# Performance work log

Hardware: AMD Instinct MI355X
Metric: run time of the kernel (lower is better)

Reference implementation:

```python
import jax, jax.numpy as jnp
import numpy as np

N, E, ND, ED, H, OUT, L, VC = 10000, 160000, 8, 4, 128, 256, 6, 6
HEADS, C = 4, 128  # GATConv: out_channels=128 per head, concat=False -> mean over heads


def _ln(x, g, b, eps=1e-5):
    m = x.mean(-1, keepdims=True)
    v = ((x - m) ** 2).mean(-1, keepdims=True)
    return (x - m) * jax.lax.rsqrt(v + eps) * g + b


def _gat_layer(h, src, dst, e_attr, lw, a_src, a_dst, lew, a_edge, bias):
    # h: [N,H]; e_attr: [Etot,H]; PyG GATConv(heads=4, concat=False, edge_dim=H)
    xh = (h @ lw).reshape(N, HEADS, C)                 # [N,4,128]
    eh = (e_attr @ lew).reshape(-1, HEADS, C)          # [Etot,4,128]
    al_s = jnp.einsum('nhc,hc->nh', xh, a_src)
    al_d = jnp.einsum('nhc,hc->nh', xh, a_dst)
    al_e = jnp.einsum('ehc,hc->eh', eh, a_edge)
    alpha = jax.nn.leaky_relu(al_s[src] + al_d[dst] + al_e, 0.2)  # [Etot,4]
    amax = jax.ops.segment_max(alpha, dst, num_segments=N)
    ex = jnp.exp(alpha - amax[dst])
    den = jax.ops.segment_sum(ex, dst, num_segments=N)
    w = ex / (den[dst] + 1e-16)
    out = jax.ops.segment_sum(xh[src] * w[..., None], dst, num_segments=N)  # [N,4,128]
    return out.mean(axis=1) + bias


def setup_inputs() -> dict:
    key = jax.random.key(0)
    ks = jax.random.split(key, 32)
    s = 0.05
    d = {
        'x': jax.random.normal(ks[0], (N, ND), jnp.float32),
        'edge_index': jax.random.randint(ks[1], (2, E), 0, N),
        'edge_attr': jax.random.uniform(ks[2], (E, ED), jnp.float32),
        'vnf_context': jax.random.normal(ks[3], (1, VC), jnp.float32),
        # node embedding
        'node_w': jax.random.normal(ks[4], (ND, H)) * s, 'node_b': jnp.zeros((H,)),
        # EdgeAttentionLayer
        'ea_proj_w': jax.random.normal(ks[5], (ED, H)) * s, 'ea_proj_b': jnp.zeros((H,)),
        'vnf_w': jax.random.normal(ks[6], (VC, H)) * s, 'vnf_b': jnp.zeros((H,)),
        'att1_w': jax.random.normal(ks[7], (2 * H, H)) * s, 'att1_b': jnp.zeros((H,)),
        'att2_w': jax.random.normal(ks[8], (H, H // 2)) * s, 'att2_b': jnp.zeros((H // 2,)),
        'att3_w': jax.random.normal(ks[9], (H // 2, 1)) * s, 'att3_b': jnp.zeros((1,)),
        # per-layer GATConv params (stacked over L layers)
        'gat_lin_w': jax.random.normal(ks[10], (L, H, HEADS * C)) * s,
        'gat_att_src': jax.random.normal(ks[11], (L, HEADS, C)) * s,
        'gat_att_dst': jax.random.normal(ks[12], (L, HEADS, C)) * s,
        'gat_lin_edge_w': jax.random.normal(ks[13], (L, H, HEADS * C)) * s,
        'gat_att_edge': jax.random.normal(ks[14], (L, HEADS, C)) * s,
        'gat_bias': jnp.zeros((L, C)),
        'ln_scale': jnp.ones((L, H)), 'ln_bias': jnp.zeros((L, H)),
        # output projection
        'out_w': jax.random.normal(ks[15], (H, OUT)) * s, 'out_b': jnp.zeros((OUT,)),
    }
    return d


def reference(x, edge_index, edge_attr, vnf_context, node_w, node_b, ea_proj_w, ea_proj_b,
              vnf_w, vnf_b, att1_w, att1_b, att2_w, att2_b, att3_w, att3_b,
              gat_lin_w, gat_att_src, gat_att_dst, gat_lin_edge_w, gat_att_edge, gat_bias,
              ln_scale, ln_bias, out_w, out_b):
    src, dst = edge_index[0], edge_index[1]
    h = x @ node_w + node_b                                   # [N,128]
    # EdgeAttentionLayer (eval mode, no network_state)
    ef = edge_attr @ ea_proj_w + ea_proj_b                    # [E,128]
    vnf = vnf_context @ vnf_w + vnf_b                         # [1,128]
    comb = jnp.concatenate([ef, jnp.broadcast_to(vnf, (E, H))], axis=-1)
    a = jax.nn.relu(comb @ att1_w + att1_b)
    a = jax.nn.relu(a @ att2_w + att2_b)
    e_gate = jax.nn.sigmoid(a @ att3_w + att3_b)              # [E,1]
    w_edge = ef * e_gate                                      # [E,128]
    # GATConv default add_self_loops=True, fill_value='mean'
    loop = jnp.arange(N)
    src2 = jnp.concatenate([src, loop])
    dst2 = jnp.concatenate([dst, loop])
    e2 = jnp.concatenate([w_edge, jnp.broadcast_to(w_edge.mean(0, keepdims=True), (N, H))], axis=0)
    for l in range(L):
        hc = _gat_layer(h, src2, dst2, e2, gat_lin_w[l], gat_att_src[l], gat_att_dst[l],
                        gat_lin_edge_w[l], gat_att_edge[l], gat_bias[l])
        h = _ln(h + jax.nn.relu(hc), ln_scale[l], ln_bias[l])
    return h @ out_w + out_b                                  # [N,256]
```

## Files before the change

kernel.cpp:

```cpp
#include <hip/hip_runtime.h>
#include <hip/hip_bf16.h>
#include <math.h>

#define Nn 10000
#define Ee 160000
#define ET 170000
#define LL 6

typedef short v8s __attribute__((ext_vector_type(8)));
typedef float v4f __attribute__((ext_vector_type(4)));
typedef float v2f __attribute__((ext_vector_type(2)));

__device__ __forceinline__ unsigned short f2bf(float v) {
    unsigned int b = __float_as_uint(v);
    b += 0x7fffu + ((b >> 16) & 1u);
    return (unsigned short)(b >> 16);
}
__device__ __forceinline__ float bflo(unsigned int u) { return __uint_as_float(u << 16); }
__device__ __forceinline__ float bfhi(unsigned int u) { return __uint_as_float(u & 0xffff0000u); }

__global__ void k_node_embed(const float* __restrict__ x, const float* __restrict__ nw,
                             const float* __restrict__ nb, float* __restrict__ h,
                             unsigned short* __restrict__ hb) {
    int idx = blockIdx.x * 256 + threadIdx.x;
    if (idx >= Nn * 128) return;
    int n = idx >> 7, c = idx & 127;
    const float* xr = x + (size_t)n * 8;
    float acc = nb[c];
#pragma unroll
    for (int k = 0; k < 8; k++) acc += xr[k] * nw[k * 128 + c];
    h[idx] = acc;
    hb[idx] = f2bf(acc);
}

__global__ void k_small(const float* __restrict__ vnfc, const float* __restrict__ vw,
                        const float* __restrict__ vb, const float* __restrict__ eab,
                        const float* __restrict__ a1w, const float* __restrict__ a1b,
                        const float* __restrict__ eaw, float* __restrict__ E1) {
    __shared__ float vr[128];
    __shared__ float sM1[512];
    __shared__ float sd1[128];
    int t = threadIdx.x;
    if (t < 128) {
        float a = vb[t];
#pragma unroll
        for (int k = 0; k < 6; k++) a += vnfc[k] * vw[k * 128 + t];
        vr[t] = a;
    }
    __syncthreads();
    if (t < 128) {
        float a = a1b[t];
        for (int k = 0; k < 128; k++) a += eab[k] * a1w[k * 128 + t];
        for (int k = 0; k < 128; k++) a += vr[k] * a1w[(128 + k) * 128 + t];
        sd1[t] = a;
    }
    {
        int r = t >> 7, j = t & 127;
        float a = 0.f;
        for (int k = 0; k < 128; k++) a += eaw[r * 128 + k] * a1w[k * 128 + j];
        sM1[r * 128 + j] = a;
    }
    __syncthreads();
    if (t < 128) {
        E1[t * 8 + 0] = sM1[t];
        E1[t * 8 + 1] = sM1[128 + t];
        E1[t * 8 + 2] = sM1[256 + t];
        E1[t * 8 + 3] = sM1[384 + t];
        E1[t * 8 + 4] = sd1[t];
        E1[t * 8 + 5] = 0.f; E1[t * 8 + 6] = 0.f; E1[t * 8 + 7] = 0.f;
    }
}

__global__ void k_bmat(const float* __restrict__ glw, const float* __restrict__ gas,
                       const float* __restrict__ gad, const float* __restrict__ glew,
                       const float* __restrict__ gae, float* __restrict__ Bs,
                       float* __restrict__ Bd, float* __restrict__ Be) {
    int idx = blockIdx.x * 256 + threadIdx.x;
    if (idx >= LL * 128 * 4) return;
    int hh = idx & 3, k = (idx >> 2) & 127, l = idx >> 9;
    const float* lwp = glw  + (size_t)l * 65536 + k * 512 + hh * 128;
    const float* lep = glew + (size_t)l * 65536 + k * 512 + hh * 128;
    const float* sp = gas + l * 512 + hh * 128;
    const float* dp = gad + l * 512 + hh * 128;
    const float* ep = gae + l * 512 + hh * 128;
    float s1 = 0, s2 = 0, s3 = 0;
    for (int c = 0; c < 128; c++) {
        float lv = lwp[c];
        s1 += lv * sp[c];
        s2 += lv * dp[c];
        s3 += lep[c] * ep[c];
    }
    Bs[idx] = s1; Bd[idx] = s2; Be[idx] = s3;
}

__global__ void k_wsum(const float* __restrict__ glw, unsigned short* __restrict__ WsumT) {
    int idx = blockIdx.x * 256 + threadIdx.x;
    if (idx >= LL * 128 * 512) return;
    int kk = idx & 511;
    int c = (idx >> 9) & 127;
    int l = idx >> 16;
    float v = 0.25f * glw[(size_t)l * 65536 + (size_t)(kk & 127) * 512 + (kk >> 7) * 128 + c];
    WsumT[(size_t)l * 65536 + (size_t)c * 512 + kk] = f2bf(v);
}

__global__ void k_pb(const float* __restrict__ eaw, const float* __restrict__ eab,
                     const float* __restrict__ Be, float* __restrict__ PB,
                     float* __restrict__ cB) {
    int t = threadIdx.x;
    if (t >= 24) return;
    int l = t >> 2, hh = t & 3;
    const float* bp = Be + l * 512 + hh;
    float s0 = 0, s1 = 0, s2 = 0, s3 = 0, sc = 0;
    for (int k = 0; k < 128; k++) {
        float bv = bp[k * 4];
        s0 += eaw[0 * 128 + k] * bv;
        s1 += eaw[1 * 128 + k] * bv;
        s2 += eaw[2 * 128 + k] * bv;
        s3 += eaw[3 * 128 + k] * bv;
        sc += eab[k] * bv;
    }
    PB[0 * 24 + t] = s0; PB[1 * 24 + t] = s1;
    PB[2 * 24 + t] = s2; PB[3 * 24 + t] = s3;
    cB[t] = sc;
}

__global__ __launch_bounds__(256, 3) void k_edge(
    const float* __restrict__ ea, const float* __restrict__ E1,
    const float* __restrict__ a2w, const float* __restrict__ a2b,
    const float* __restrict__ a3w, const float* __restrict__ a3b,
    float* __restrict__ Gg, float4* __restrict__ Ge4, float* __restrict__ gsum) {
    __shared__ float sw2[128 * 64];
    __shared__ float4 sM[128];
    __shared__ float sD[128];
    __shared__ float prs[4][256];
    __shared__ float gsh[256];
    int t = threadIdx.x;
    int lane = t & 63;
    int p = t >> 6;
    int ps = __builtin_amdgcn_readfirstlane(p);
    for (int z = t; z < 2048; z += 256) ((float4*)sw2)[z] = ((const float4*)a2w)[z];
    if (t < 128) { sM[t] = *(const float4*)(E1 + t * 8); sD[t] = E1[t * 8 + 4]; }
    __syncthreads();
    int eb = blockIdx.x * 256 + lane;
    float4 ev[4];
#pragma unroll
    for (int r = 0; r < 4; r++) ev[r] = *(const float4*)(ea + (size_t)(eb + r * 64) * 4);
    v2f acc[4][8];
#pragma unroll
    for (int j = 0; j < 8; j++) {
        v2f b = {a2b[ps * 16 + 2 * j], a2b[ps * 16 + 2 * j + 1]};
#pragma unroll
        for (int r = 0; r < 4; r++) acc[r][j] = b;
    }
    const float* w2base = sw2 + ps * 16;
    for (int k = 0; k < 128; k++) {
        float4 m = sM[k];
        float dk = sD[k];
        v2f xx[4];
#pragma unroll
        for (int r = 0; r < 4; r++) {
            float xv = fmaxf(dk + ev[r].x * m.x + ev[r].y * m.y + ev[r].z * m.z + ev[r].w * m.w, 0.f);
            xx[r][0] = xv; xx[r][1] = xv;
        }
        const float* w2r = w2base + k * 64;
#pragma unroll
        for (int j4 = 0; j4 < 4; j4++) {
            float4 wv = *(const float4*)(w2r + j4 * 4);
            v2f w01 = {wv.x, wv.y}, w23 = {wv.z, wv.w};
#pragma unroll
            for (int r = 0; r < 4; r++) {
                acc[r][2 * j4]     += xx[r] * w01;
                acc[r][2 * j4 + 1] += xx[r] * w23;
            }
        }
    }
#pragma unroll
    for (int r = 0; r < 4; r++) {
        float pr = 0.f;
#pragma unroll
        for (int j = 0; j < 8; j++) {
            pr += fmaxf(acc[r][j][0], 0.f) * a3w[ps * 16 + 2 * j];
            pr += fmaxf(acc[r][j][1], 0.f) * a3w[ps * 16 + 2 * j + 1];
        }
        prs[p][r * 64 + lane] = pr;
    }
    __syncthreads();
    if (p == 0) {
        float v0 = 0.f, v1 = 0.f, v2 = 0.f, v3 = 0.f, v4 = 0.f;
#pragma unroll
        for (int rep = 0; rep < 4; rep++) {
            int le = rep * 64 + lane;
            float tot = prs[0][le] + prs[1][le] + prs[2][le] + prs[3][le] + a3b[0];
            float g = 1.f / (1.f + __expf(-tot));
            gsh[le] = g;
            float4 evv = ev[rep];
            v0 += g; v1 += g * evv.x; v2 += g * evv.y; v3 += g * evv.z; v4 += g * evv.w;
        }
#pragma unroll
        for (int d = 32; d > 0; d >>= 1) {
            v0 += __shfl_down(v0, d); v1 += __shfl_down(v1, d); v2 += __shfl_down(v2, d);
            v3 += __shfl_down(v3, d); v4 += __shfl_down(v4, d);
        }
        if (lane == 0) {
            atomicAdd(&gsum[0], v0); atomicAdd(&gsum[1], v1); atomicAdd(&gsum[2], v2);
            atomicAdd(&gsum[3], v3); atomicAdd(&gsum[4], v4);
        }
    }
    __syncthreads();
    {
        int e = blockIdx.x * 256 + ps * 64 + lane;
        float g = gsh[ps * 64 + lane];
        float4 evv = *(const float4*)(ea + (size_t)e * 4);
        Gg[e] = g;
        Ge4[e] = make_float4(g * evv.x, g * evv.y, g * evv.z, g * evv.w);
    }
}

__global__ void k_hist(const int* __restrict__ ei, int* __restrict__ hist) {
    int i = blockIdx.x * 256 + threadIdx.x;
    if (i >= ET) return;
    int d = (i < Ee) ? ei[Ee + i] : (i - Ee);
    atomicAdd(&hist[d], 1);
}

__global__ __launch_bounds__(1024) void k_scan(const int* __restrict__ hist,
                                               int* __restrict__ seg, int* __restrict__ pos) {
    __shared__ int wsums[16];
    __shared__ int carry_s;
    int t = threadIdx.x;
    int lane = t & 63, wid = t >> 6;
    if (t == 0) { carry_s = 0; seg[0] = 0; }
    __syncthreads();
    for (int base = 0; base < Nn; base += 1024) {
        int idx = base + t;
        int v = (idx < Nn) ? hist[idx] : 0;
        int sc = v;
#pragma unroll
        for (int d = 1; d < 64; d <<= 1) {
            int up = __shfl_up(sc, d);
            if (lane >= d) sc += up;
        }
        if (lane == 63) wsums[wid] = sc;
        __syncthreads();
        if (wid == 0) {
            int wv = (lane < 16) ? wsums[lane] : 0;
            int wsc = wv;
#pragma unroll
            for (int d = 1; d < 16; d <<= 1) {
                int up = __shfl_up(wsc, d);
                if (lane >= d) wsc += up;
            }
            if (lane < 16) wsums[lane] = wsc - wv;
        }
        __syncthreads();
        int carry = carry_s;
        int inc = sc + wsums[wid] + carry;
        if (idx < Nn) { seg[idx + 1] = inc; pos[idx] = inc - v; }
        __syncthreads();
        if (t == 1023) carry_s = inc;
        __syncthreads();
    }
}

__global__ void k_scatter(const int* __restrict__ ei, int* __restrict__ pos,
                          int2* __restrict__ pse) {
    int i = blockIdx.x * 256 + threadIdx.x;
    if (i >= ET) return;
    int s, d;
    if (i < Ee) { s = ei[i]; d = ei[Ee + i]; } else { s = d = i - Ee; }
    int idx = atomicAdd(&pos[d], 1);
    pse[idx] = make_int2(s, i);
}

__global__ void k_ales(const int2* __restrict__ pse, const float* __restrict__ Gg,
                       const float4* __restrict__ Ge4, const float* __restrict__ gsum,
                       const float* __restrict__ PB, const float* __restrict__ cB,
                       float4* __restrict__ aleS) {
    int i = blockIdx.x * 256 + threadIdx.x;
    if (i >= ET) return;
    int y = pse[i].y;
    float g;
    float4 ge;
    if (y < Ee) { g = Gg[y]; ge = Ge4[y]; }
    else {
        float inv = 1.f / Ee;
        g = gsum[0] * inv;
        ge = make_float4(gsum[1] * inv, gsum[2] * inv, gsum[3] * inv, gsum[4] * inv);
    }
#pragma unroll
    for (int l = 0; l < LL; l++) {
        float4 o;
        o.x = g * cB[l * 4 + 0] + ge.x * PB[0 * 24 + l * 4 + 0] + ge.y * PB[1 * 24 + l * 4 + 0]
            + ge.z * PB[2 * 24 + l * 4 + 0] + ge.w * PB[3 * 24 + l * 4 + 0];
        o.y = g * cB[l * 4 + 1] + ge.x * PB[0 * 24 + l * 4 + 1] + ge.y * PB[1 * 24 + l * 4 + 1]
            + ge.z * PB[2 * 24 + l * 4 + 1] + ge.w * PB[3 * 24 + l * 4 + 1];
        o.z = g * cB[l * 4 + 2] + ge.x * PB[0 * 24 + l * 4 + 2] + ge.y * PB[1 * 24 + l * 4 + 2]
            + ge.z * PB[2 * 24 + l * 4 + 2] + ge.w * PB[3 * 24 + l * 4 + 2];
        o.w = g * cB[l * 4 + 3] + ge.x * PB[0 * 24 + l * 4 + 3] + ge.y * PB[1 * 24 + l * 4 + 3]
            + ge.z * PB[2 * 24 + l * 4 + 3] + ge.w * PB[3 * 24 + l * 4 + 3];
        aleS[(size_t)l * ET + i] = o;
    }
}

__global__ void k_ab(const float* __restrict__ h, const float* __restrict__ Bs_l,
                     const float* __restrict__ Bd_l, float* __restrict__ als,
                     float* __restrict__ ald) {
    int idx = blockIdx.x * 256 + threadIdx.x;
    if (idx >= Nn * 8) return;
    int n = idx >> 3, slot = idx & 7;
    const float* B = (slot < 4) ? Bs_l : Bd_l;
    int hh = slot & 3;
    const float4* hr = (const float4*)(h + (size_t)n * 128);
    float s = 0.f;
#pragma unroll 8
    for (int kb = 0; kb < 32; kb++) {
        float4 hv = hr[kb];
        s += hv.x * B[(4 * kb + 0) * 4 + hh] + hv.y * B[(4 * kb + 1) * 4 + hh]
           + hv.z * B[(4 * kb + 2) * 4 + hh] + hv.w * B[(4 * kb + 3) * 4 + hh];
    }
    if (slot < 4) als[n * 4 + hh] = s;
    else          ald[n * 4 + hh] = s;
}

__global__ __launch_bounds__(256) void k_agg4(
    const int2* __restrict__ pse, const int* __restrict__ seg,
    const float* __restrict__ als, const float* __restrict__ ald,
    const float4* __restrict__ aleS_l, const unsigned short* __restrict__ hb,
    unsigned short* __restrict__ aggb) {
    __shared__ float part[3][512];
    __shared__ float pden[3][4];
    int t = threadIdx.x;
    int lane = t & 63;
    int wv = t >> 6;
    int n = blockIdx.x;
    int start = seg[n], end = seg[n + 1];
    int deg = end - start;
    int quarter = (deg + 3) >> 2;
    int s0 = start + wv * quarter;
    int e0 = min(s0 + quarter, end);
    int hp = lane >> 4;
    int cch = (lane & 15) * 8;
    float aldh = ald[n * 4 + hp];
    float den = 0.f;
    float4 acc0 = make_float4(0.f, 0.f, 0.f, 0.f);
    float4 acc1 = make_float4(0.f, 0.f, 0.f, 0.f);
    int i = s0;
    for (; i + 2 <= e0; i += 2) {
        int sa = pse[i].x, sb = pse[i + 1].x;
        float4 ala4 = aleS_l[i], alb4 = aleS_l[i + 1];
        float ala = hp == 0 ? ala4.x : hp == 1 ? ala4.y : hp == 2 ? ala4.z : ala4.w;
        float alb = hp == 0 ? alb4.x : hp == 1 ? alb4.y : hp == 2 ? alb4.z : alb4.w;
        float ava = als[sa * 4 + hp] + aldh + ala;
        float avb = als[sb * 4 + hp] + aldh + alb;
        ava = ava > 0.f ? ava : 0.2f * ava;
        avb = avb > 0.f ? avb : 0.2f * avb;
        float ea = __expf(fminf(ava, 60.f));
        float eb = __expf(fminf(avb, 60.f));
        den += ea + eb;
        uint4 ua = *(const uint4*)(hb + (size_t)sa * 128 + cch);
        uint4 ub = *(const uint4*)(hb + (size_t)sb * 128 + cch);
        acc0.x += ea * bflo(ua.x) + eb * bflo(ub.x);
        acc0.y += ea * bfhi(ua.x) + eb * bfhi(ub.x);
        acc0.z += ea * bflo(ua.y) + eb * bflo(ub.y);
        acc0.w += ea * bfhi(ua.y) + eb * bfhi(ub.y);
        acc1.x += ea * bflo(ua.z) + eb * bflo(ub.z);
        acc1.y += ea * bfhi(ua.z) + eb * bfhi(ub.z);
        acc1.z += ea * bflo(ua.w) + eb * bflo(ub.w);
        acc1.w += ea * bfhi(ua.w) + eb * bfhi(ub.w);
    }
    if (i < e0) {
        int sa = pse[i].x;
        float4 ala4 = aleS_l[i];
        float ala = hp == 0 ? ala4.x : hp == 1 ? ala4.y : hp == 2 ? ala4.z : ala4.w;
        float ava = als[sa * 4 + hp] + aldh + ala;
        ava = ava > 0.f ? ava : 0.2f * ava;
        float ea = __expf(fminf(ava, 60.f));
        den += ea;
        uint4 ua = *(const uint4*)(hb + (size_t)sa * 128 + cch);
        acc0.x += ea * bflo(ua.x); acc0.y += ea * bfhi(ua.x);
        acc0.z += ea * bflo(ua.y); acc0.w += ea * bfhi(ua.y);
        acc1.x += ea * bflo(ua.z); acc1.y += ea * bfhi(ua.z);
        acc1.z += ea * bflo(ua.w); acc1.w += ea * bfhi(ua.w);
    }
    if (wv > 0) {
        *(float4*)&part[wv - 1][lane * 8] = acc0;
        *(float4*)&part[wv - 1][lane * 8 + 4] = acc1;
        if ((lane & 15) == 0) pden[wv - 1][hp] = den;
    }
    __syncthreads();
    if (wv == 0) {
        float dtot = den + pden[0][hp] + pden[1][hp] + pden[2][hp];
#pragma unroll
        for (int r = 0; r < 3; r++) {
            float4 p0 = *(const float4*)&part[r][lane * 8];
            float4 p1 = *(const float4*)&part[r][lane * 8 + 4];
            acc0.x += p0.x; acc0.y += p0.y; acc0.z += p0.z; acc0.w += p0.w;
            acc1.x += p1.x; acc1.y += p1.y; acc1.z += p1.z; acc1.w += p1.w;
        }
        float inv = 1.f / (dtot + 1e-16f);
        acc0.x *= inv; acc0.y *= inv; acc0.z *= inv; acc0.w *= inv;
        acc1.x *= inv; acc1.y *= inv; acc1.z *= inv; acc1.w *= inv;
        ushort4 q0, q1;
        q0.x = f2bf(acc0.x); q0.y = f2bf(acc0.y); q0.z = f2bf(acc0.z); q0.w = f2bf(acc0.w);
        q1.x = f2bf(acc1.x); q1.y = f2bf(acc1.y); q1.z = f2bf(acc1.z); q1.w = f2bf(acc1.w);
        *(ushort4*)(aggb + (size_t)n * 512 + lane * 8) = q0;
        *(ushort4*)(aggb + (size_t)n * 512 + lane * 8 + 4) = q1;
    }
}

__global__ __launch_bounds__(256) void k_post(
    const unsigned short* __restrict__ aggb, const unsigned short* __restrict__ WsumT_l,
    const float* __restrict__ gbias, const float* __restrict__ lnsc,
    const float* __restrict__ lnbi, float* __restrict__ h,
    unsigned short* __restrict__ hb, const float* __restrict__ Bs_n,
    const float* __restrict__ Bd_n, float* __restrict__ als, float* __restrict__ ald) {
    int t = threadIdx.x;
    int lane = t & 63, w = t >> 6;
    int n0 = (blockIdx.x * 4 + w) * 16;
    if (n0 >= Nn) return;
    int m = lane & 15, q = lane >> 4;
    v4f acc[8];
#pragma unroll
    for (int nt = 0; nt < 8; nt++) acc[nt] = (v4f){0.f, 0.f, 0.f, 0.f};
    const unsigned short* arow = aggb + (size_t)(n0 + m) * 512 + q * 8;
#pragma unroll 4
    for (int ks = 0; ks < 16; ks++) {
        v8s fa = *(const v8s*)(arow + ks * 32);
#pragma unroll
        for (int nt = 0; nt < 8; nt++) {
            int col = nt * 16 + m;
            v8s fb = *(const v8s*)(WsumT_l + (size_t)col * 512 + ks * 32 + q * 8);
            acc[nt] = __builtin_amdgcn_mfma_f32_16x16x32_bf16(fa, fb, acc[nt], 0, 0, 0);
        }
    }
    float v[8][4];
    float s1[4] = {0.f, 0.f, 0.f, 0.f}, s2[4] = {0.f, 0.f, 0.f, 0.f};
#pragma unroll
    for (int nt = 0; nt < 8; nt++) {
        int col = nt * 16 + m;
        float b = gbias[col];
#pragma unroll
        for (int r = 0; r < 4; r++) {
            int row = n0 + q * 4 + r;
            float val = h[(size_t)row * 128 + col] + fmaxf(acc[nt][r] + b, 0.f);
            v[nt][r] = val;
            s1[r] += val; s2[r] += val * val;
        }
    }
#pragma unroll
    for (int d = 1; d <= 8; d <<= 1) {
#pragma unroll
        for (int r = 0; r < 4; r++) {
            s1[r] += __shfl_xor(s1[r], d);
            s2[r] += __shfl_xor(s2[r], d);
        }
    }
    float o8[8][4];
#pragma unroll
    for (int r = 0; r < 4; r++) {
        float mean = s1[r] * (1.f / 128.f);
        float var = s2[r] * (1.f / 128.f) - mean * mean;
        float rinv = rsqrtf(var + 1e-5f);
        int row = n0 + q * 4 + r;
#pragma unroll
        for (int nt = 0; nt < 8; nt++) {
            int col = nt * 16 + m;
            float o = (v[nt][r] - mean) * rinv * lnsc[col] + lnbi[col];
            o8[nt][r] = o;
            h[(size_t)row * 128 + col] = o;
            hb[(size_t)row * 128 + col] = f2bf(o);
        }
    }
    float sal[4][4], sad[4][4];
#pragma unroll
    for (int r = 0; r < 4; r++) {
#pragma unroll
        for (int hh = 0; hh < 4; hh++) { sal[r][hh] = 0.f; sad[r][hh] = 0.f; }
    }
#pragma unroll
    for (int nt = 0; nt < 8; nt++) {
        int col = nt * 16 + m;
        float4 bs = *(const float4*)(Bs_n + col * 4);
        float4 bd = *(const float4*)(Bd_n + col * 4);
#pragma unroll
        for (int r = 0; r < 4; r++) {
            float o = o8[nt][r];
            sal[r][0] += o * bs.x; sal[r][1] += o * bs.y;
            sal[r][2] += o * bs.z; sal[r][3] += o * bs.w;
            sad[r][0] += o * bd.x; sad[r][1] += o * bd.y;
            sad[r][2] += o * bd.z; sad[r][3] += o * bd.w;
        }
    }
#pragma unroll
    for (int d = 1; d <= 8; d <<= 1) {
#pragma unroll
        for (int r = 0; r < 4; r++) {
#pragma unroll
            for (int hh = 0; hh < 4; hh++) {
                sal[r][hh] += __shfl_xor(sal[r][hh], d);
                sad[r][hh] += __shfl_xor(sad[r][hh], d);
            }
        }
    }
    if (m < 8) {
        int hh = m & 3;
#pragma unroll
        for (int r = 0; r < 4; r++) {
            int row = n0 + q * 4 + r;
            float va = (hh == 0) ? sal[r][0] : (hh == 1) ? sal[r][1] : (hh == 2) ? sal[r][2] : sal[r][3];
            float vd = (hh == 0) ? sad[r][0] : (hh == 1) ? sad[r][1] : (hh == 2) ? sad[r][2] : sad[r][3];
            if (m < 4) als[row * 4 + hh] = va;
            else       ald[row * 4 + hh] = vd;
        }
    }
}

__global__ __launch_bounds__(256) void k_out(
    const float* __restrict__ h, const float* __restrict__ ow,
    const float* __restrict__ ob, float* __restrict__ out) {
    __shared__ float4 hs4[8][32];
    int t = threadIdx.x;
    int n0 = blockIdx.x * 8;
    if (t < 256) {
        int i = t >> 5, kb = t & 31;
        hs4[i][kb] = *(const float4*)(h + (size_t)(n0 + i) * 128 + 4 * kb);
    }
    __syncthreads();
    float acc[8] = {0, 0, 0, 0, 0, 0, 0, 0};
    for (int kb = 0; kb < 32; kb++) {
        float w0 = ow[(4 * kb + 0) * 256 + t];
        float w1 = ow[(4 * kb + 1) * 256 + t];
        float w2 = ow[(4 * kb + 2) * 256 + t];
        float w3 = ow[(4 * kb + 3) * 256 + t];
#pragma unroll
        for (int i = 0; i < 8; i++) {
            float4 hv = hs4[i][kb];
            acc[i] += hv.x * w0 + hv.y * w1 + hv.z * w2 + hv.w * w3;
        }
    }
    float b = ob[t];
#pragma unroll
    for (int i = 0; i < 8; i++) out[(size_t)(n0 + i) * 256 + t] = acc[i] + b;
}

extern "C" void kernel_launch(void* const* d_in, const int* in_sizes, int n_in,
                              void* d_out, int out_size, void* d_ws, size_t ws_size,
                              hipStream_t stream) {
    const float* x    = (const float*)d_in[0];
    const int*   ei   = (const int*)d_in[1];
    const float* ea   = (const float*)d_in[2];
    const float* vnfc = (const float*)d_in[3];
    const float* nw   = (const float*)d_in[4];
    const float* nb   = (const float*)d_in[5];
    const float* eaw  = (const float*)d_in[6];
    const float* eab  = (const float*)d_in[7];
    const float* vw   = (const float*)d_in[8];
    const float* vb   = (const float*)d_in[9];
    const float* a1w  = (const float*)d_in[10];
    const float* a1b  = (const float*)d_in[11];
    const float* a2w  = (const float*)d_in[12];
    const float* a2b  = (const float*)d_in[13];
    const float* a3w  = (const float*)d_in[14];
    const float* a3b  = (const float*)d_in[15];
    const float* glw  = (const float*)d_in[16];
    const float* gas  = (const float*)d_in[17];
    const float* gad  = (const float*)d_in[18];
    const float* glew = (const float*)d_in[19];
    const float* gae  = (const float*)d_in[20];
    const float* gb   = (const float*)d_in[21];
    const float* lnsc = (const float*)d_in[22];
    const float* lnbi = (const float*)d_in[23];
    const float* ow   = (const float*)d_in[24];
    const float* ob   = (const float*)d_in[25];
    float* out = (float*)d_out;

    char* w = (char*)d_ws;
    size_t o = 0;
    auto allocf = [&](size_t cnt) { float* p = (float*)(w + o); o += ((cnt * 4 + 255) / 256) * 256; return p; };
    auto alloci = [&](size_t cnt) { int* p = (int*)(w + o); o += ((cnt * 4 + 255) / 256) * 256; return p; };
    auto allocu = [&](size_t cnt) { unsigned short* p = (unsigned short*)(w + o); o += ((cnt * 2 + 255) / 256) * 256; return p; };
    float* h      = allocf((size_t)Nn * 128);
    unsigned short* hb    = allocu((size_t)Nn * 128);
    unsigned short* aggb  = allocu((size_t)Nn * 512);
    unsigned short* WsumT = allocu((size_t)LL * 128 * 512);
    float* als    = allocf((size_t)Nn * 4);
    float* ald    = allocf((size_t)Nn * 4);
    float* Gg     = allocf((size_t)Ee);
    float4* Ge4   = (float4*)allocf((size_t)Ee * 4);
    float4* aleS  = (float4*)allocf((size_t)LL * ET * 4);
    float* Bs     = allocf(3072);
    float* Bd     = allocf(3072);
    float* Be     = allocf(3072);
    float* E1     = allocf(1024);
    float* PB     = allocf(96);
    float* cB     = allocf(24);
    float* gsum   = allocf(8);
    int* seg  = alloci(Nn + 1);
    int* hist = alloci(Nn);
    int* pos  = alloci(Nn);
    int2* pse = (int2*)alloci((size_t)ET * 2);

    hipMemsetAsync(hist, 0, Nn * sizeof(int), stream);
    hipMemsetAsync(gsum, 0, 8 * sizeof(float), stream);

    k_node_embed<<<(Nn * 128 + 255) / 256, 256, 0, stream>>>(x, nw, nb, h, hb);
    k_small<<<1, 512, 0, stream>>>(vnfc, vw, vb, eab, a1w, a1b, eaw, E1);
    k_bmat<<<(LL * 128 * 4 + 255) / 256, 256, 0, stream>>>(glw, gas, gad, glew, gae, Bs, Bd, Be);
    k_wsum<<<(LL * 128 * 512 + 255) / 256, 256, 0, stream>>>(glw, WsumT);
    k_pb<<<1, 32, 0, stream>>>(eaw, eab, Be, PB, cB);
    k_edge<<<Ee / 256, 256, 0, stream>>>(ea, E1, a2w, a2b, a3w, a3b, Gg, Ge4, gsum);
    k_hist<<<(ET + 255) / 256, 256, 0, stream>>>(ei, hist);
    k_scan<<<1, 1024, 0, stream>>>(hist, seg, pos);
    k_scatter<<<(ET + 255) / 256, 256, 0, stream>>>(ei, pos, pse);
    k_ales<<<(ET + 255) / 256, 256, 0, stream>>>(pse, Gg, Ge4, gsum, PB, cB, aleS);
    k_ab<<<(Nn * 8 + 255) / 256, 256, 0, stream>>>(h, Bs, Bd, als, ald);
    for (int l = 0; l < LL; l++) {
        int ln = (l + 1) % LL;
        k_agg4<<<Nn, 256, 0, stream>>>(pse, seg, als, ald, aleS + (size_t)l * ET, hb, aggb);
        k_post<<<(625 + 3) / 4, 256, 0, stream>>>(aggb, WsumT + (size_t)l * 65536,
                                                  gb + l * 128, lnsc + l * 128, lnbi + l * 128,
                                                  h, hb, Bs + ln * 512, Bd + ln * 512, als, ald);
    }
    k_out<<<Nn / 8, 256, 0, stream>>>(h, ow, ob, out);
}
```

Before: 564.2 us.

## Spread edge MLP and post-GEMM work across more waves per block

```diff
diff --git a/kernel.cpp b/kernel.cpp
--- a/kernel.cpp
+++ b/kernel.cpp
@@ -124,7 +124,7 @@
     cB[t] = sc;
 }
 
-__global__ __launch_bounds__(256, 3) void k_edge(
+__global__ __launch_bounds__(512, 6) void k_edge(
     const float* __restrict__ ea, const float* __restrict__ E1,
     const float* __restrict__ a2w, const float* __restrict__ a2b,
     const float* __restrict__ a3w, const float* __restrict__ a3b,
@@ -136,64 +136,59 @@
     __shared__ float gsh[256];
     int t = threadIdx.x;
     int lane = t & 63;
-    int p = t >> 6;
-    int ps = __builtin_amdgcn_readfirstlane(p);
-    for (int z = t; z < 2048; z += 256) ((float4*)sw2)[z] = ((const float4*)a2w)[z];
+    int w = t >> 6;
+    int jq = __builtin_amdgcn_readfirstlane(w & 3);
+    int eh = __builtin_amdgcn_readfirstlane(w >> 2);
+    for (int z = t; z < 2048; z += 512) ((float4*)sw2)[z] = ((const float4*)a2w)[z];
     if (t < 128) { sM[t] = *(const float4*)(E1 + t * 8); sD[t] = E1[t * 8 + 4]; }
     __syncthreads();
-    int eb = blockIdx.x * 256 + lane;
-    float4 ev[4];
-#pragma unroll
-    for (int r = 0; r < 4; r++) ev[r] = *(const float4*)(ea + (size_t)(eb + r * 64) * 4);
-    v2f acc[4][8];
+    int e0 = blockIdx.x * 256 + eh * 128 + lane;
+    float4 ev0 = *(const float4*)(ea + (size_t)e0 * 4);
+    float4 ev1 = *(const float4*)(ea + (size_t)(e0 + 64) * 4);
+    v2f acc[2][8];
 #pragma unroll
     for (int j = 0; j < 8; j++) {
-        v2f b = {a2b[ps * 16 + 2 * j], a2b[ps * 16 + 2 * j + 1]};
-#pragma unroll
-        for (int r = 0; r < 4; r++) acc[r][j] = b;
-    }
-    const float* w2base = sw2 + ps * 16;
+        v2f b = {a2b[jq * 16 + 2 * j], a2b[jq * 16 + 2 * j + 1]};
+        acc[0][j] = b; acc[1][j] = b;
+    }
+    const float* w2base = sw2 + jq * 16;
     for (int k = 0; k < 128; k++) {
         float4 m = sM[k];
         float dk = sD[k];
-        v2f xx[4];
-#pragma unroll
-        for (int r = 0; r < 4; r++) {
-            float xv = fmaxf(dk + ev[r].x * m.x + ev[r].y * m.y + ev[r].z * m.z + ev[r].w * m.w, 0.f);
-            xx[r][0] = xv; xx[r][1] = xv;
-        }
+        float x0 = fmaxf(dk + ev0.x * m.x + ev0.y * m.y + ev0.z * m.z + ev0.w * m.w, 0.f);
+        float x1 = fmaxf(dk + ev1.x * m.x + ev1.y * m.y + ev1.z * m.z + ev1.w * m.w, 0.f);
+        v2f xx0 = {x0, x0}, xx1 = {x1, x1};
         const float* w2r = w2base + k * 64;
 #pragma unroll
         for (int j4 = 0; j4 < 4; j4++) {
             float4 wv = *(const float4*)(w2r + j4 * 4);
             v2f w01 = {wv.x, wv.y}, w23 = {wv.z, wv.w};
-#pragma unroll
-            for (int r = 0; r < 4; r++) {
-                acc[r][2 * j4]     += xx[r] * w01;
-                acc[r][2 * j4 + 1] += xx[r] * w23;
-            }
-        }
-    }
-#pragma unroll
-    for (int r = 0; r < 4; r++) {
+            acc[0][2 * j4]     += xx0 * w01;
+            acc[0][2 * j4 + 1] += xx0 * w23;
+            acc[1][2 * j4]     += xx1 * w01;
+            acc[1][2 * j4 + 1] += xx1 * w23;
+        }
+    }
+#pragma unroll
+    for (int r = 0; r < 2; r++) {
         float pr = 0.f;
 #pragma unroll
         for (int j = 0; j < 8; j++) {
-            pr += fmaxf(acc[r][j][0], 0.f) * a3w[ps * 16 + 2 * j];
-            pr += fmaxf(acc[r][j][1], 0.f) * a3w[ps * 16 + 2 * j + 1];
-        }
-        prs[p][r * 64 + lane] = pr;
-    }
-    __syncthreads();
-    if (p == 0) {
+            pr += fmaxf(acc[r][j][0], 0.f) * a3w[jq * 16 + 2 * j];
+            pr += fmaxf(acc[r][j][1], 0.f) * a3w[jq * 16 + 2 * j + 1];
+        }
+        prs[jq][eh * 128 + r * 64 + lane] = pr;
+    }
+    __syncthreads();
+    if ((w & 3) == 0) {
         float v0 = 0.f, v1 = 0.f, v2 = 0.f, v3 = 0.f, v4 = 0.f;
 #pragma unroll
-        for (int rep = 0; rep < 4; rep++) {
-            int le = rep * 64 + lane;
+        for (int rep = 0; rep < 2; rep++) {
+            int le = eh * 128 + rep * 64 + lane;
             float tot = prs[0][le] + prs[1][le] + prs[2][le] + prs[3][le] + a3b[0];
             float g = 1.f / (1.f + __expf(-tot));
             gsh[le] = g;
-            float4 evv = ev[rep];
+            float4 evv = rep == 0 ? ev0 : ev1;
             v0 += g; v1 += g * evv.x; v2 += g * evv.y; v3 += g * evv.z; v4 += g * evv.w;
         }
 #pragma unroll
@@ -207,9 +202,9 @@
         }
     }
     __syncthreads();
-    {
-        int e = blockIdx.x * 256 + ps * 64 + lane;
-        float g = gsh[ps * 64 + lane];
+    if (w < 4) {
+        int e = blockIdx.x * 256 + w * 64 + lane;
+        float g = gsh[w * 64 + lane];
         float4 evv = *(const float4*)(ea + (size_t)e * 4);
         Gg[e] = g;
         Ge4[e] = make_float4(g * evv.x, g * evv.y, g * evv.z, g * evv.w);
@@ -414,36 +409,36 @@
     const float* __restrict__ lnbi, float* __restrict__ h,
     unsigned short* __restrict__ hb, const float* __restrict__ Bs_n,
     const float* __restrict__ Bd_n, float* __restrict__ als, float* __restrict__ ald) {
+    __shared__ float sred1[4][16], sred2[4][16];
+    __shared__ float sA[4][16][4], sDd[4][16][4];
     int t = threadIdx.x;
     int lane = t & 63, w = t >> 6;
-    int n0 = (blockIdx.x * 4 + w) * 16;
-    if (n0 >= Nn) return;
+    int n0 = blockIdx.x * 16;
     int m = lane & 15, q = lane >> 4;
-    v4f acc[8];
-#pragma unroll
-    for (int nt = 0; nt < 8; nt++) acc[nt] = (v4f){0.f, 0.f, 0.f, 0.f};
+    v4f acc[2];
+    acc[0] = (v4f){0.f, 0.f, 0.f, 0.f};
+    acc[1] = (v4f){0.f, 0.f, 0.f, 0.f};
     const unsigned short* arow = aggb + (size_t)(n0 + m) * 512 + q * 8;
+    int col0 = (2 * w) * 16 + m, col1 = (2 * w + 1) * 16 + m;
 #pragma unroll 4
     for (int ks = 0; ks < 16; ks++) {
         v8s fa = *(const v8s*)(arow + ks * 32);
-#pragma unroll
-        for (int nt = 0; nt < 8; nt++) {
-            int col = nt * 16 + m;
-            v8s fb = *(const v8s*)(WsumT_l + (size_t)col * 512 + ks * 32 + q * 8);
-            acc[nt] = __builtin_amdgcn_mfma_f32_16x16x32_bf16(fa, fb, acc[nt], 0, 0, 0);
-        }
-    }
-    float v[8][4];
+        v8s fb0 = *(const v8s*)(WsumT_l + (size_t)col0 * 512 + ks * 32 + q * 8);
+        v8s fb1 = *(const v8s*)(WsumT_l + (size_t)col1 * 512 + ks * 32 + q * 8);
+        acc[0] = __builtin_amdgcn_mfma_f32_16x16x32_bf16(fa, fb0, acc[0], 0, 0, 0);
+        acc[1] = __builtin_amdgcn_mfma_f32_16x16x32_bf16(fa, fb1, acc[1], 0, 0, 0);
+    }
+    float v[2][4];
     float s1[4] = {0.f, 0.f, 0.f, 0.f}, s2[4] = {0.f, 0.f, 0.f, 0.f};
 #pragma unroll
-    for (int nt = 0; nt < 8; nt++) {
-        int col = nt * 16 + m;
+    for (int j = 0; j < 2; j++) {
+        int col = j == 0 ? col0 : col1;
         float b = gbias[col];
 #pragma unroll
         for (int r = 0; r < 4; r++) {
             int row = n0 + q * 4 + r;
-            float val = h[(size_t)row * 128 + col] + fmaxf(acc[nt][r] + b, 0.f);
-            v[nt][r] = val;
+            float val = h[(size_t)row * 128 + col] + fmaxf(acc[j][r] + b, 0.f);
+            v[j][r] = val;
             s1[r] += val; s2[r] += val * val;
         }
     }
@@ -455,36 +450,43 @@
             s2[r] += __shfl_xor(s2[r], d);
         }
     }
-    float o8[8][4];
+    if (m == 0) {
+#pragma unroll
+        for (int r = 0; r < 4; r++) { sred1[w][q * 4 + r] = s1[r]; sred2[w][q * 4 + r] = s2[r]; }
+    }
+    __syncthreads();
+    float o2[2][4];
 #pragma unroll
     for (int r = 0; r < 4; r++) {
-        float mean = s1[r] * (1.f / 128.f);
-        float var = s2[r] * (1.f / 128.f) - mean * mean;
+        int row = q * 4 + r;
+        float t1 = sred1[0][row] + sred1[1][row] + sred1[2][row] + sred1[3][row];
+        float t2 = sred2[0][row] + sred2[1][row] + sred2[2][row] + sred2[3][row];
+        float mean = t1 * (1.f / 128.f);
+        float var = t2 * (1.f / 128.f) - mean * mean;
         float rinv = rsqrtf(var + 1e-5f);
-        int row = n0 + q * 4 + r;
-#pragma unroll
-        for (int nt = 0; nt < 8; nt++) {
-            int col = nt * 16 + m;
-            float o = (v[nt][r] - mean) * rinv * lnsc[col] + lnbi[col];
-            o8[nt][r] = o;
-            h[(size_t)row * 128 + col] = o;
-            hb[(size_t)row * 128 + col] = f2bf(o);
+        int grow = n0 + row;
+#pragma unroll
+        for (int j = 0; j < 2; j++) {
+            int col = j == 0 ? col0 : col1;
+            float o = (v[j][r] - mean) * rinv * lnsc[col] + lnbi[col];
+            o2[j][r] = o;
+            h[(size_t)grow * 128 + col] = o;
+            hb[(size_t)grow * 128 + col] = f2bf(o);
         }
     }
     float sal[4][4], sad[4][4];
 #pragma unroll
-    for (int r = 0; r < 4; r++) {
+    for (int r = 0; r < 4; r++)
 #pragma unroll
         for (int hh = 0; hh < 4; hh++) { sal[r][hh] = 0.f; sad[r][hh] = 0.f; }
-    }
-#pragma unroll
-    for (int nt = 0; nt < 8; nt++) {
-        int col = nt * 16 + m;
+#pragma unroll
+    for (int j = 0; j < 2; j++) {
+        int col = j == 0 ? col0 : col1;
         float4 bs = *(const float4*)(Bs_n + col * 4);
         float4 bd = *(const float4*)(Bd_n + col * 4);
 #pragma unroll
         for (int r = 0; r < 4; r++) {
-            float o = o8[nt][r];
+            float o = o2[j][r];
             sal[r][0] += o * bs.x; sal[r][1] += o * bs.y;
             sal[r][2] += o * bs.z; sal[r][3] += o * bs.w;
             sad[r][0] += o * bd.x; sad[r][1] += o * bd.y;
@@ -494,23 +496,31 @@
 #pragma unroll
     for (int d = 1; d <= 8; d <<= 1) {
 #pragma unroll
-        for (int r = 0; r < 4; r++) {
+        for (int r = 0; r < 4; r++)
 #pragma unroll
             for (int hh = 0; hh < 4; hh++) {
                 sal[r][hh] += __shfl_xor(sal[r][hh], d);
                 sad[r][hh] += __shfl_xor(sad[r][hh], d);
             }
-        }
-    }
-    if (m < 8) {
-        int hh = m & 3;
-#pragma unroll
-        for (int r = 0; r < 4; r++) {
-            int row = n0 + q * 4 + r;
-            float va = (hh == 0) ? sal[r][0] : (hh == 1) ? sal[r][1] : (hh == 2) ? sal[r][2] : sal[r][3];
-            float vd = (hh == 0) ? sad[r][0] : (hh == 1) ? sad[r][1] : (hh == 2) ? sad[r][2] : sad[r][3];
-            if (m < 4) als[row * 4 + hh] = va;
-            else       ald[row * 4 + hh] = vd;
+    }
+    if (m == 0) {
+#pragma unroll
+        for (int r = 0; r < 4; r++)
+#pragma unroll
+            for (int hh = 0; hh < 4; hh++) {
+                sA[w][q * 4 + r][hh] = sal[r][hh];
+                sDd[w][q * 4 + r][hh] = sad[r][hh];
+            }
+    }
+    __syncthreads();
+    if (t < 128) {
+        int row = t >> 3, slot = t & 7, hh = slot & 3;
+        if (slot < 4) {
+            float va = sA[0][row][hh] + sA[1][row][hh] + sA[2][row][hh] + sA[3][row][hh];
+            als[(n0 + row) * 4 + hh] = va;
+        } else {
+            float vd = sDd[0][row][hh] + sDd[1][row][hh] + sDd[2][row][hh] + sDd[3][row][hh];
+            ald[(n0 + row) * 4 + hh] = vd;
         }
     }
 }
@@ -608,7 +618,7 @@
     k_bmat<<<(LL * 128 * 4 + 255) / 256, 256, 0, stream>>>(glw, gas, gad, glew, gae, Bs, Bd, Be);
     k_wsum<<<(LL * 128 * 512 + 255) / 256, 256, 0, stream>>>(glw, WsumT);
     k_pb<<<1, 32, 0, stream>>>(eaw, eab, Be, PB, cB);
-    k_edge<<<Ee / 256, 256, 0, stream>>>(ea, E1, a2w, a2b, a3w, a3b, Gg, Ge4, gsum);
+    k_edge<<<Ee / 256, 512, 0, stream>>>(ea, E1, a2w, a2b, a3w, a3b, Gg, Ge4, gsum);
     k_hist<<<(ET + 255) / 256, 256, 0, stream>>>(ei, hist);
     k_scan<<<1, 1024, 0, stream>>>(hist, seg, pos);
     k_scatter<<<(ET + 255) / 256, 256, 0, stream>>>(ei, pos, pse);
@@ -617,9 +627,9 @@
     for (int l = 0; l < LL; l++) {
         int ln = (l + 1) % LL;
         k_agg4<<<Nn, 256, 0, stream>>>(pse, seg, als, ald, aleS + (size_t)l * ET, hb, aggb);
-        k_post<<<(625 + 3) / 4, 256, 0, stream>>>(aggb, WsumT + (size_t)l * 65536,
-                                                  gb + l * 128, lnsc + l * 128, lnbi + l * 128,
-                                                  h, hb, Bs + ln * 512, Bd + ln * 512, als, ald);
+        k_post<<<625, 256, 0, stream>>>(aggb, WsumT + (size_t)l * 65536,
+                                        gb + l * 128, lnsc + l * 128, lnbi + l * 128,
+                                        h, hb, Bs + ln * 512, Bd + ln * 512, als, ald);
     }
     k_out<<<Nn / 8, 256, 0, stream>>>(h, ow, ob, out);
 }
```

New measurement: 607.8 us. +7.7%, slower.
